# Optimization experiments

Measured on AMD Instinct MI355X. Metric: run time of the kernel, lower is better.

## Reference

```python
import jax, jax.numpy as jnp
import numpy as np

B, N, D_U = 32, 4096, 64
D = 128          # mlp_dim == model dim after MLP
H = 2            # n_heads
DH = D // H


def setup_inputs() -> dict:
    key = jax.random.key(0)
    ks = jax.random.split(key, 16)
    sc = lambda fan_in: 1.0 / np.sqrt(fan_in)
    inp = {
        "u": jax.random.normal(ks[0], (B, N, D_U), dtype=jnp.float32),
        "x": jax.random.uniform(ks[1], (B, N, 2), dtype=jnp.float32),
        # MLP params: [D_U -> D -> D], gelu after each hidden layer
        "W1": jax.random.normal(ks[2], (D_U, D), dtype=jnp.float32) * sc(D_U),
        "b1": jnp.zeros((D,), jnp.float32),
        "W2": jax.random.normal(ks[3], (D, D), dtype=jnp.float32) * sc(D),
        "b2": jnp.zeros((D,), jnp.float32),
        # learned pooling query (nn.Embed(1, D))
        "embed": jax.random.normal(ks[4], (1, D), dtype=jnp.float32),
        # multihead linear attention projections
        "Wq": jax.random.normal(ks[5], (D, D), dtype=jnp.float32) * sc(D),
        "bq": jnp.zeros((D,), jnp.float32),
        "Wk": jax.random.normal(ks[6], (D, D), dtype=jnp.float32) * sc(D),
        "bk": jnp.zeros((D,), jnp.float32),
        "Wv": jax.random.normal(ks[7], (D, D), dtype=jnp.float32) * sc(D),
        "bv": jnp.zeros((D,), jnp.float32),
        "Wo": jax.random.normal(ks[8], (D, D), dtype=jnp.float32) * sc(D),
        "bo": jnp.zeros((D,), jnp.float32),
    }
    return inp


def reference(u, x, W1, b1, W2, b2, embed, Wq, bq, Wk, bk, Wv, bv, Wo, bo):
    # MLP on set elements: [B, N, D_U] -> [B, N, D]
    z = jax.nn.gelu(u @ W1 + b1)
    z = jax.nn.gelu(z @ W2 + b2)

    n = z.shape[1]
    # learned query broadcast over batch: [B, 1, D]
    s = jnp.broadcast_to(embed[None, :, :], (z.shape[0], 1, z.shape[-1]))

    # multihead linear (Galerkin-style, softmax-free) attention
    q = (s @ Wq + bq).reshape(z.shape[0], 1, H, DH)   # [B, 1, H, DH]
    k = (z @ Wk + bk).reshape(z.shape[0], n, H, DH)   # [B, N, H, DH]
    v = (z @ Wv + bv).reshape(z.shape[0], n, H, DH)   # [B, N, H, DH]

    # context = K^T V / N per head: [B, H, DH, DH]
    context = jnp.einsum("bnhd,bnhe->bhde", k, v) / n
    out = jnp.einsum("bqhd,bhde->bqhe", q, context)   # [B, 1, H, DH]
    out = out.reshape(z.shape[0], 1, D) @ Wo + bo     # [B, 1, D]

    return out[:, 0, :]                               # [B, D]
```

## Files before the change

kernel.cpp:

```cpp
#include <hip/hip_runtime.h>
#include <math.h>

#define Bsz 32
#define Nn  4096
#define DU  64
#define Dm  128

#define GRID_MLP 512

#define WS_WKQ 0
#define WS_BKQ 256
#define WS_CNT 288
#define WS_A   320
#define WS_S   384
#define WS_WP  8576
#define WS_M   20864
#define WS_VB  53632

#define H1STR 136

typedef short frag_ab __attribute__((ext_vector_type(8)));
typedef float frag_cd __attribute__((ext_vector_type(4)));

__device__ __forceinline__ unsigned short f2bf(float x) {
    union { float f; unsigned int u; } c; c.f = x;
    unsigned int r = c.u + 0x7fffu + ((c.u >> 16) & 1u);
    return (unsigned short)(r >> 16);
}

__device__ __forceinline__ float gelu_fast(float x) {
    float t = x * x;
    float a = x * fmaf(t, -0.1029432f, -2.3022081f);
    float e = __builtin_amdgcn_exp2f(a);
    return x * __builtin_amdgcn_rcpf(1.0f + e);
}

__global__ __launch_bounds__(256) void precompute_kernel(
    const float* __restrict__ embed, const float* __restrict__ Wq,
    const float* __restrict__ bq, const float* __restrict__ Wk,
    const float* __restrict__ bk, const float* __restrict__ W1,
    const float* __restrict__ W2, const float* __restrict__ Wv,
    const float* __restrict__ bv, const float* __restrict__ Wo,
    float* __restrict__ ws)
{
    __shared__ float qv[128];
    __shared__ float pp[256];
    const int tid = threadIdx.x;
    const int bid = blockIdx.x;

    if (bid < 12) {
        const int e = bid * 256 + tid;
        const int f = e >> 6, L = e & 63;
        const int q2 = L >> 4, n = L & 15;
        const float* src;
        int ks, nt;
        if (f < 16) { src = W1; ks = f >> 3;        nt = f & 7; }
        else        { src = W2; ks = (f - 16) >> 3; nt = (f - 16) & 7; }
        const int kb = ks * 32 + q2 * 8;
        const int c  = nt * 16 + n;
        unsigned int p[4];
        #pragma unroll
        for (int jj = 0; jj < 4; ++jj) {
            unsigned int lo = f2bf(src[(kb + 2 * jj)     * Dm + c]);
            unsigned int hi = f2bf(src[(kb + 2 * jj + 1) * Dm + c]);
            p[jj] = lo | (hi << 16);
        }
        ((uint4*)(ws + WS_WP))[e] = make_uint4(p[0], p[1], p[2], p[3]);
    } else if (bid == 12) {
        const int c = tid & 127, sg = tid >> 7;
        {
            float s = 0.f;
            #pragma unroll 8
            for (int j0 = 0; j0 < 64; ++j0) {
                const int j = sg * 64 + j0;
                s += embed[j] * Wq[j * 128 + c];
            }
            pp[tid] = s;
        }
        __syncthreads();
        if (tid < 128) qv[tid] = bq[tid] + pp[tid] + pp[128 + tid];
        __syncthreads();
        {
            float s = 0.f;
            #pragma unroll 8
            for (int dh = 0; dh < 64; ++dh)
                s += Wk[c * 128 + sg * 64 + dh] * qv[sg * 64 + dh];
            ws[WS_WKQ + sg * 128 + c] = s;
        }
        if (tid < 2) {
            float s = 0.f;
            for (int dh = 0; dh < 64; ++dh) s += bk[tid * 64 + dh] * qv[tid * 64 + dh];
            ws[WS_BKQ + tid] = s;
        }
    } else if (bid == 13) {
        for (int idx = WS_CNT + tid; idx < WS_WP; idx += 256) ws[idx] = 0.f;
    } else if (bid < 30) {
        const int base = (bid - 14) * 256 + tid;
        #pragma unroll
        for (int k = 0; k < 8; ++k) {
            const int o  = base + 4096 * k;
            const int hd = o >> 7, i = o & 127;
            const int h = hd >> 7, d = hd & 127;
            float acc = 0.f;
            #pragma unroll 8
            for (int c64 = 0; c64 < 64; ++c64)
                acc += Wv[d * 128 + h * 64 + c64] * Wo[(h * 64 + c64) * 128 + i];
            ws[WS_M + o] = acc * (1.0f / 4096.0f);
        }
    } else {
        if (tid < 256) {
            const int h = tid >> 7, i = tid & 127;
            float acc = 0.f;
            #pragma unroll 8
            for (int c64 = 0; c64 < 64; ++c64)
                acc += bv[h * 64 + c64] * Wo[(h * 64 + c64) * 128 + i];
            ws[WS_VB + tid] = acc * (1.0f / 4096.0f);
        }
    }
}

__global__ __launch_bounds__(512) void mlp_pool_kernel(
    const float* __restrict__ u,  const float* __restrict__ b1,
    const float* __restrict__ b2, float* __restrict__ ws)
{
    __shared__ short lds_w[48 * 512];
    __shared__ short lds_h1[4 * 16 * H1STR];
    __shared__ float a2buf[4][16][2][2];
    __shared__ float b1_lds[128];

    const int tid  = threadIdx.x;
    const int wave = tid >> 6;
    const int lane = tid & 63;
    const int quad = lane >> 4;
    const int n15  = lane & 15;
    const int p    = wave >> 1;
    const int hf   = wave & 1;

    {
        const float4* src = (const float4*)(ws + WS_WP);
        float4* dst = (float4*)lds_w;
        #pragma unroll
        for (int i = 0; i < 6; ++i) dst[tid + 512 * i] = src[tid + 512 * i];
        if (tid < 128) b1_lds[tid] = b1[tid];
    }

    float b2c[4], wkq0[4], wkq1[4];
    #pragma unroll
    for (int nt = 0; nt < 4; ++nt) {
        const int c = hf * 64 + nt * 16 + n15;
        b2c[nt]  = b2[c];
        wkq0[nt] = ws[WS_WKQ + c];
        wkq1[nt] = ws[WS_WKQ + 128 + c];
    }
    const float bkq0 = ws[WS_BKQ];
    const float bkq1 = ws[WS_BKQ + 1];
    __syncthreads();

    const int bb = blockIdx.x >> 4;
    const int jb = blockIdx.x & 15;
    short* h1t = lds_h1 + p * 16 * H1STR;

    float s0p[4], s1p[4];
    #pragma unroll
    for (int nt = 0; nt < 4; ++nt) { s0p[nt] = 0.f; s1p[nt] = 0.f; }
    float aA0 = 0.f, aA1 = 0.f;

    const float* ub = u + ((size_t)(bb * Nn + jb * 256 + p * 16 + n15)) * DU + quad * 8;
    float4 f0 = *(const float4*)(ub);
    float4 f1 = *(const float4*)(ub + 4);
    float4 f2 = *(const float4*)(ub + 32);
    float4 f3 = *(const float4*)(ub + 36);

    #pragma unroll 1
    for (int it = 0; it < 4; ++it) {
        frag_ab a0, a1;
        a0[0] = (short)f2bf(f0.x); a0[1] = (short)f2bf(f0.y);
        a0[2] = (short)f2bf(f0.z); a0[3] = (short)f2bf(f0.w);
        a0[4] = (short)f2bf(f1.x); a0[5] = (short)f2bf(f1.y);
        a0[6] = (short)f2bf(f1.z); a0[7] = (short)f2bf(f1.w);
        a1[0] = (short)f2bf(f2.x); a1[1] = (short)f2bf(f2.y);
        a1[2] = (short)f2bf(f2.z); a1[3] = (short)f2bf(f2.w);
        a1[4] = (short)f2bf(f3.x); a1[5] = (short)f2bf(f3.y);
        a1[6] = (short)f2bf(f3.z); a1[7] = (short)f2bf(f3.w);

        #pragma unroll
        for (int i = 0; i < 4; ++i) {
            const int ct = hf * 4 + i;
            float4 bi = *(const float4*)&b1_lds[ct * 16 + quad * 4];
            frag_cd acc = (frag_cd){bi.x, bi.y, bi.z, bi.w};
            frag_ab w0 = *(const frag_ab*)&lds_w[(ct)     * 512 + lane * 8];
            acc = __builtin_amdgcn_mfma_f32_16x16x32_bf16(w0, a0, acc, 0, 0, 0);
            frag_ab w1 = *(const frag_ab*)&lds_w[(8 + ct) * 512 + lane * 8];
            acc = __builtin_amdgcn_mfma_f32_16x16x32_bf16(w1, a1, acc, 0, 0, 0);
            unsigned int lo = (unsigned int)f2bf(gelu_fast(acc[0]))
                            | ((unsigned int)f2bf(gelu_fast(acc[1])) << 16);
            unsigned int hi = (unsigned int)f2bf(gelu_fast(acc[2]))
                            | ((unsigned int)f2bf(gelu_fast(acc[3])) << 16);
            *(uint2*)&h1t[n15 * H1STR + ct * 16 + quad * 4] = make_uint2(lo, hi);
        }
        __syncthreads();

        if (it < 3) {
            const float* un = ub + (size_t)((it + 1) * 64) * DU;
            f0 = *(const float4*)(un);
            f1 = *(const float4*)(un + 4);
            f2 = *(const float4*)(un + 32);
            f3 = *(const float4*)(un + 36);
        }

        frag_cd acc2[4];
        #pragma unroll
        for (int nt = 0; nt < 4; ++nt)
            acc2[nt] = (frag_cd){b2c[nt], b2c[nt], b2c[nt], b2c[nt]};
        #pragma unroll
        for (int ks = 0; ks < 4; ++ks) {
            frag_ab a2 = *(const frag_ab*)&h1t[n15 * H1STR + ks * 32 + quad * 8];
            #pragma unroll
            for (int nt = 0; nt < 4; ++nt) {
                frag_ab w2f = *(const frag_ab*)&lds_w[(16 + ks * 8 + hf * 4 + nt) * 512 + lane * 8];
                acc2[nt] = __builtin_amdgcn_mfma_f32_16x16x32_bf16(a2, w2f, acc2[nt], 0, 0, 0);
            }
        }

        #pragma unroll
        for (int nt = 0; nt < 4; ++nt) {
            #pragma unroll
            for (int r = 0; r < 4; ++r)
                acc2[nt][r] = gelu_fast(acc2[nt][r]);
        }

        float p0[4], p1[4];
        #pragma unroll
        for (int r = 0; r < 4; ++r) { p0[r] = 0.f; p1[r] = 0.f; }
        #pragma unroll
        for (int nt = 0; nt < 4; ++nt) {
            #pragma unroll
            for (int r = 0; r < 4; ++r) {
                p0[r] += acc2[nt][r] * wkq0[nt];
                p1[r] += acc2[nt][r] * wkq1[nt];
            }
        }
        #pragma unroll
        for (int r = 0; r < 4; ++r) {
            #pragma unroll
            for (int d = 1; d < 16; d <<= 1) {
                p0[r] += __shfl_xor(p0[r], d);
                p1[r] += __shfl_xor(p1[r], d);
            }
        }
        if (n15 == 0) {
            #pragma unroll
            for (int r = 0; r < 4; ++r) {
                const int row = quad * 4 + r;
                a2buf[p][row][0][hf] = p0[r];
                a2buf[p][row][1][hf] = p1[r];
            }
        }
        __syncthreads();

        #pragma unroll
        for (int r = 0; r < 4; ++r) {
            const int row = quad * 4 + r;
            const float al0 = a2buf[p][row][0][0] + a2buf[p][row][0][1] + bkq0;
            const float al1 = a2buf[p][row][1][0] + a2buf[p][row][1][1] + bkq1;
            #pragma unroll
            for (int nt = 0; nt < 4; ++nt) {
                s0p[nt] += al0 * acc2[nt][r];
                s1p[nt] += al1 * acc2[nt][r];
            }
            aA0 += al0; aA1 += al1;
        }
    }

    #pragma unroll
    for (int nt = 0; nt < 4; ++nt) {
        s0p[nt] += __shfl_xor(s0p[nt], 16); s0p[nt] += __shfl_xor(s0p[nt], 32);
        s1p[nt] += __shfl_xor(s1p[nt], 16); s1p[nt] += __shfl_xor(s1p[nt], 32);
    }
    aA0 += __shfl_xor(aA0, 16); aA0 += __shfl_xor(aA0, 32);
    aA1 += __shfl_xor(aA1, 16); aA1 += __shfl_xor(aA1, 32);

    if (quad == 0) {
        #pragma unroll
        for (int nt = 0; nt < 4; ++nt) {
            const int c = hf * 64 + nt * 16 + n15;
            atomicAdd(&ws[WS_S + (bb * 2 + 0) * 128 + c], s0p[nt]);
            atomicAdd(&ws[WS_S + (bb * 2 + 1) * 128 + c], s1p[nt]);
        }
    }
    if (hf == 0 && lane == 0) {
        atomicAdd(&ws[WS_A + bb * 2 + 0], aA0);
        atomicAdd(&ws[WS_A + bb * 2 + 1], aA1);
    }
}

__global__ __launch_bounds__(512) void pool_out_kernel(
    const float* __restrict__ bo, const float* __restrict__ ws,
    float* __restrict__ out)
{
    __shared__ float sS[256];
    __shared__ float sA[2];
    __shared__ float part[512];

    const int bb  = blockIdx.x;
    const int tid = threadIdx.x;

    if (tid < 256) sS[tid] = ws[WS_S + bb * 256 + tid];
    else if (tid < 258) sA[tid - 256] = ws[WS_A + bb * 2 + (tid - 256)];
    __syncthreads();

    const int i = tid & 127, seg = tid >> 7;
    float acc = 0.f;
    #pragma unroll 8
    for (int k = 0; k < 64; ++k) {
        const int hd = seg * 64 + k;
        acc += sS[hd] * ws[WS_M + hd * 128 + i];
    }
    part[tid] = acc;
    __syncthreads();

    if (tid < 128)
        out[bb * 128 + tid] = bo[tid]
            + part[tid] + part[128 + tid] + part[256 + tid] + part[384 + tid]
            + sA[0] * ws[WS_VB + tid] + sA[1] * ws[WS_VB + 128 + tid];
}

extern "C" void kernel_launch(void* const* d_in, const int* in_sizes, int n_in,
                              void* d_out, int out_size, void* d_ws, size_t ws_size,
                              hipStream_t stream) {
    const float* u     = (const float*)d_in[0];
    const float* W1    = (const float*)d_in[2];
    const float* b1    = (const float*)d_in[3];
    const float* W2    = (const float*)d_in[4];
    const float* b2    = (const float*)d_in[5];
    const float* embed = (const float*)d_in[6];
    const float* Wq    = (const float*)d_in[7];
    const float* bq    = (const float*)d_in[8];
    const float* Wk    = (const float*)d_in[9];
    const float* bk    = (const float*)d_in[10];
    const float* Wv    = (const float*)d_in[11];
    const float* bv    = (const float*)d_in[12];
    const float* Wo    = (const float*)d_in[13];
    const float* bo    = (const float*)d_in[14];
    float* ws  = (float*)d_ws;
    float* out = (float*)d_out;

    hipLaunchKernelGGL(precompute_kernel, dim3(31), dim3(256), 0, stream,
                       embed, Wq, bq, Wk, bk, W1, W2, Wv, bv, Wo, ws);
    hipLaunchKernelGGL(mlp_pool_kernel, dim3(GRID_MLP), dim3(512), 0, stream,
                       u, b1, b2, ws);
    hipLaunchKernelGGL(pool_out_kernel, dim3(Bsz), dim3(512), 0, stream,
                       bo, ws, out);
}
```

Measured before the change: 152.8 us.

## Fuse output projection into MLP-pool kernel and drop the third launch

```diff
diff --git a/kernel.cpp b/kernel.cpp
--- a/kernel.cpp
+++ b/kernel.cpp
@@ -11,8 +11,6 @@
 #define WS_WKQ 0
 #define WS_BKQ 256
 #define WS_CNT 288
-#define WS_A   320
-#define WS_S   384
 #define WS_WP  8576
 #define WS_M   20864
 #define WS_VB  53632
@@ -41,7 +39,8 @@
     const float* __restrict__ bk, const float* __restrict__ W1,
     const float* __restrict__ W2, const float* __restrict__ Wv,
     const float* __restrict__ bv, const float* __restrict__ Wo,
-    float* __restrict__ ws)
+    const float* __restrict__ bo, float* __restrict__ ws,
+    float* __restrict__ out)
 {
     __shared__ float qv[128];
     __shared__ float pp[256];
@@ -107,7 +106,7 @@
                 acc += Wv[d * 128 + h * 64 + c64] * Wo[(h * 64 + c64) * 128 + i];
             ws[WS_M + o] = acc * (1.0f / 4096.0f);
         }
-    } else {
+    } else if (bid == 30) {
         if (tid < 256) {
             const int h = tid >> 7, i = tid & 127;
             float acc = 0.f;
@@ -116,12 +115,15 @@
                 acc += bv[h * 64 + c64] * Wo[(h * 64 + c64) * 128 + i];
             ws[WS_VB + tid] = acc * (1.0f / 4096.0f);
         }
+    } else {
+        for (int o = tid; o < Bsz * 128; o += 256) out[o] = bo[o & 127];
     }
 }
 
 __global__ __launch_bounds__(512) void mlp_pool_kernel(
     const float* __restrict__ u,  const float* __restrict__ b1,
-    const float* __restrict__ b2, float* __restrict__ ws)
+    const float* __restrict__ b2, float* __restrict__ ws,
+    float* __restrict__ out)
 {
     __shared__ short lds_w[48 * 512];
     __shared__ short lds_h1[4 * 16 * H1STR];
@@ -280,49 +282,45 @@
     aA0 += __shfl_xor(aA0, 16); aA0 += __shfl_xor(aA0, 32);
     aA1 += __shfl_xor(aA1, 16); aA1 += __shfl_xor(aA1, 32);
 
+    float* sw   = (float*)lds_h1;
+    float* aw   = sw + 1024;
+    float* Sb   = sw + 1032;
+    float* part = sw + 1288;
+
     if (quad == 0) {
         #pragma unroll
         for (int nt = 0; nt < 4; ++nt) {
             const int c = hf * 64 + nt * 16 + n15;
-            atomicAdd(&ws[WS_S + (bb * 2 + 0) * 128 + c], s0p[nt]);
-            atomicAdd(&ws[WS_S + (bb * 2 + 1) * 128 + c], s1p[nt]);
-        }
-    }
-    if (hf == 0 && lane == 0) {
-        atomicAdd(&ws[WS_A + bb * 2 + 0], aA0);
-        atomicAdd(&ws[WS_A + bb * 2 + 1], aA1);
-    }
-}
-
-__global__ __launch_bounds__(512) void pool_out_kernel(
-    const float* __restrict__ bo, const float* __restrict__ ws,
-    float* __restrict__ out)
-{
-    __shared__ float sS[256];
-    __shared__ float sA[2];
-    __shared__ float part[512];
-
-    const int bb  = blockIdx.x;
-    const int tid = threadIdx.x;
-
-    if (tid < 256) sS[tid] = ws[WS_S + bb * 256 + tid];
-    else if (tid < 258) sA[tid - 256] = ws[WS_A + bb * 2 + (tid - 256)];
+            sw[p * 256 + c]       = s0p[nt];
+            sw[p * 256 + 128 + c] = s1p[nt];
+        }
+        if (hf == 0 && lane == 0) { aw[p * 2] = aA0; aw[p * 2 + 1] = aA1; }
+    }
     __syncthreads();
 
-    const int i = tid & 127, seg = tid >> 7;
-    float acc = 0.f;
-    #pragma unroll 8
-    for (int k = 0; k < 64; ++k) {
-        const int hd = seg * 64 + k;
-        acc += sS[hd] * ws[WS_M + hd * 128 + i];
-    }
-    part[tid] = acc;
+    if (tid < 256)
+        Sb[tid] = sw[tid] + sw[256 + tid] + sw[512 + tid] + sw[768 + tid];
     __syncthreads();
 
-    if (tid < 128)
-        out[bb * 128 + tid] = bo[tid]
-            + part[tid] + part[128 + tid] + part[256 + tid] + part[384 + tid]
-            + sA[0] * ws[WS_VB + tid] + sA[1] * ws[WS_VB + 128 + tid];
+    {
+        const int i = tid & 127, seg = tid >> 7;
+        float acc = 0.f;
+        #pragma unroll 8
+        for (int k = 0; k < 64; ++k) {
+            const int hd = seg * 64 + k;
+            acc += Sb[hd] * ws[WS_M + hd * 128 + i];
+        }
+        part[tid] = acc;
+    }
+    __syncthreads();
+
+    if (tid < 128) {
+        const float aT0 = aw[0] + aw[2] + aw[4] + aw[6];
+        const float aT1 = aw[1] + aw[3] + aw[5] + aw[7];
+        atomicAdd(&out[bb * 128 + tid],
+                  part[tid] + part[128 + tid] + part[256 + tid] + part[384 + tid]
+                  + aT0 * ws[WS_VB + tid] + aT1 * ws[WS_VB + 128 + tid]);
+    }
 }
 
 extern "C" void kernel_launch(void* const* d_in, const int* in_sizes, int n_in,
@@ -345,10 +343,8 @@
     float* ws  = (float*)d_ws;
     float* out = (float*)d_out;
 
-    hipLaunchKernelGGL(precompute_kernel, dim3(31), dim3(256), 0, stream,
-                       embed, Wq, bq, Wk, bk, W1, W2, Wv, bv, Wo, ws);
+    hipLaunchKernelGGL(precompute_kernel, dim3(32), dim3(256), 0, stream,
+                       embed, Wq, bq, Wk, bk, W1, W2, Wv, bv, Wo, bo, ws, out);
     hipLaunchKernelGGL(mlp_pool_kernel, dim3(GRID_MLP), dim3(512), 0, stream,
-                       u, b1, b2, ws);
-    hipLaunchKernelGGL(pool_out_kernel, dim3(Bsz), dim3(512), 0, stream,
-                       bo, ws, out);
-}
+                       u, b1, b2, ws, out);
+}
```

Result: faster. 132.7 us (-13.2%).
